# Kernel optimization log

Measured on AMD Instinct MI355X. Metric: run time of the kernel, lower is better.

Reference implementation:

```python
import jax, jax.numpy as jnp
import numpy as np

N = 50000
E = 800000
NODE_F = 128
HID = 96
TEMP_F = 10


def setup_inputs() -> dict:
    key = jax.random.key(0)
    ks = jax.random.split(key, 10)
    x = jax.random.normal(ks[0], (N, NODE_F), dtype=jnp.float32)
    edge_index = jax.random.randint(ks[1], (2, E), 0, N, dtype=jnp.int64)
    temporal = jax.random.normal(ks[2], (N, TEMP_F), dtype=jnp.float32)
    # GCNConv: lin weight [in, out] (no bias in lin), separate bias [out]
    W_gcn = jax.random.normal(ks[3], (NODE_F, HID), dtype=jnp.float32) / np.sqrt(NODE_F)
    b_gcn = jnp.zeros((HID,), dtype=jnp.float32)
    W1 = jax.random.normal(ks[4], (HID + TEMP_F, HID), dtype=jnp.float32) / np.sqrt(HID + TEMP_F)
    b1 = jax.random.normal(ks[5], (HID,), dtype=jnp.float32) * 0.01
    W2 = jax.random.normal(ks[6], (HID + NODE_F, 1), dtype=jnp.float32) / np.sqrt(HID + NODE_F)
    b2 = jax.random.normal(ks[7], (1,), dtype=jnp.float32) * 0.01
    return {"x": x, "edge_index": edge_index, "temporal": temporal,
            "W_gcn": W_gcn, "b_gcn": b_gcn, "W1": W1, "b1": b1, "W2": W2, "b2": b2}


def _gcn_conv(x, edge_index, W, b):
    n = x.shape[0]
    loop = jnp.arange(n, dtype=edge_index.dtype)
    src = jnp.concatenate([edge_index[0], loop])  # [E+N]
    dst = jnp.concatenate([edge_index[1], loop])
    # symmetric normalization with self-loops (PyG gcn_norm)
    ones = jnp.ones(src.shape[0], dtype=x.dtype)
    deg = jax.ops.segment_sum(ones, dst, num_segments=n)
    dinv = jnp.where(deg > 0, jax.lax.rsqrt(deg), 0.0)
    norm = dinv[src] * dinv[dst]  # [E+N]
    h = x @ W  # [N, HID]
    msg = h[src] * norm[:, None]  # [E+N, HID] gather + scale
    out = jax.ops.segment_sum(msg, dst, num_segments=n)  # scatter-add
    return out + b


def reference(x, edge_index, temporal, W_gcn, b_gcn, W1, b1, W2, b2):
    h = jax.nn.relu(_gcn_conv(x, edge_index, W_gcn, b_gcn))  # [N, HID]
    h = jnp.concatenate([h, temporal], axis=-1)              # [N, HID+TEMP_F]
    h = jax.nn.relu(h @ W1 + b1)                             # [N, HID]
    h = jnp.concatenate([h, x], axis=-1)                     # [N, HID+NODE_F]
    return jax.nn.relu(h @ W2 + b2)                          # [N, 1]
```

## Files before the change

### kernel.cpp

```cpp
#include <hip/hip_runtime.h>
#include <hip/hip_bf16.h>

#define NN 50000
#define NPAD 50048
#define NE 800000
#define NF 128
#define HH 96
#define TF 10
#define Z1DIM (HH + TF)
#define ZK 128
#define NCH 4
#define CW 24
#define NBK 196
#define CAP 5120
#define EPB 4096
#define FILLA_B ((NE + EPB - 1) / EPB)

typedef __attribute__((ext_vector_type(8))) short short8;
typedef __attribute__((ext_vector_type(8))) unsigned short ushort8;
typedef __attribute__((ext_vector_type(4))) float f32x4;

__device__ __forceinline__ float bu2f(unsigned short u) {
    union { unsigned int i; float f; } c;
    c.i = ((unsigned int)u) << 16;
    return c.f;
}
__device__ __forceinline__ unsigned short f2bu(float f) {
    union { __hip_bfloat16 h; unsigned short u; } c;
    c.h = __float2bfloat16(f);
    return c.u;
}

__global__ void k_init(int* __restrict__ bcur, int* __restrict__ off) {
    int t = threadIdx.x;
    if (t < NBK) bcur[t] = t * CAP;
    if (t == 255) off[NN] = NE;
}

#define WBLK (NF * HH / 4 / 256)
#define W1BLK (HH * ZK / 4 / 256)
#define ZTBLK (NPAD / 32)
#define ZPBLK 5
__global__ __launch_bounds__(256) void k_pre(const int* __restrict__ ei,
                                             int* __restrict__ bcur,
                                             int* __restrict__ temp,
                                             const float* __restrict__ W,
                                             const float* __restrict__ W1,
                                             const float* __restrict__ tmp,
                                             unsigned short* __restrict__ Wt,
                                             unsigned short* __restrict__ Wt1,
                                             unsigned short* __restrict__ zb) {
    const int t = threadIdx.x;
    if (blockIdx.x < FILLA_B) {
        __shared__ int hist[NBK], bas[NBK];
        for (int m = t; m < NBK; m += 256) hist[m] = 0;
        __syncthreads();
        const int e0 = blockIdx.x * EPB;
        const int ecap = min(e0 + EPB, NE);
        for (int e = e0 + t; e < ecap; e += 256) {
            int d = ei[NE + e];
            atomicAdd(&hist[d >> 8], 1);
        }
        __syncthreads();
        for (int m = t; m < NBK; m += 256) {
            int c = hist[m];
            bas[m] = c ? atomicAdd(&bcur[m], c) : 0;
            hist[m] = 0;
        }
        __syncthreads();
        for (int e = e0 + t; e < ecap; e += 256) {
            int d = ei[NE + e], s = ei[e];
            int b = d >> 8;
            int r = atomicAdd(&hist[b], 1);
            temp[bas[b] + r] = ((d & 255) << 16) | s;
        }
        return;
    }
    int b = blockIdx.x - FILLA_B;
    if (b < WBLK) {
        int e = (b * 256 + t) * 4;
        int n = e >> 7, k = e & 127;
        ushort4 v;
        v.x = f2bu(W[(k + 0) * HH + n]);
        v.y = f2bu(W[(k + 1) * HH + n]);
        v.z = f2bu(W[(k + 2) * HH + n]);
        v.w = f2bu(W[(k + 3) * HH + n]);
        *(ushort4*)(Wt + e) = v;
    } else if (b < WBLK + W1BLK) {
        int e = ((b - WBLK) * 256 + t) * 4;
        int n = e >> 7, k = e & 127;
        ushort4 v;
        v.x = (k + 0 < Z1DIM) ? f2bu(W1[(k + 0) * HH + n]) : (unsigned short)0;
        v.y = (k + 1 < Z1DIM) ? f2bu(W1[(k + 1) * HH + n]) : (unsigned short)0;
        v.z = (k + 2 < Z1DIM) ? f2bu(W1[(k + 2) * HH + n]) : (unsigned short)0;
        v.w = (k + 3 < Z1DIM) ? f2bu(W1[(k + 3) * HH + n]) : (unsigned short)0;
        *(ushort4*)(Wt1 + e) = v;
    } else if (b < WBLK + W1BLK + ZTBLK) {
        int t4 = ((b - WBLK - W1BLK) * 256 + t) * 4;
        int i = t4 >> 5, cc = t4 & 31;
        ushort4 v; v.x = v.y = v.z = v.w = 0;
        if (i < NN) {
            if (cc + 0 < TF) v.x = f2bu(tmp[(size_t)i * TF + cc + 0]);
            if (cc + 1 < TF) v.y = f2bu(tmp[(size_t)i * TF + cc + 1]);
            if (cc + 2 < TF) v.z = f2bu(tmp[(size_t)i * TF + cc + 2]);
            if (cc + 3 < TF) v.w = f2bu(tmp[(size_t)i * TF + cc + 3]);
        }
        *(ushort4*)(zb + (size_t)i * ZK + HH + cc) = v;
    } else {
        int t4 = ((b - WBLK - W1BLK - ZTBLK) * 256 + t) * 4;
        if (t4 < (NPAD - NN) * HH) {
            int i = NN + t4 / HH, j = t4 % HH;
            ushort4 z; z.x = z.y = z.z = z.w = 0;
            *(ushort4*)(zb + (size_t)i * ZK + j) = z;
        }
    }
}

__global__ __launch_bounds__(256) void k_off(const int* __restrict__ temp,
                                             const int* __restrict__ bcur,
                                             int* __restrict__ off) {
    __shared__ int ls[256], lc[256];
    const int b = blockIdx.x, t = threadIdx.x;
    int szt = (t < NBK) ? (bcur[t] - t * CAP) : 0;
    ls[t] = szt;
    __syncthreads();
#pragma unroll
    for (int d = 1; d < 256; d <<= 1) {
        int u = (t >= d) ? ls[t - d] : 0;
        __syncthreads();
        ls[t] += u;
        __syncthreads();
    }
    const int g0 = (b > 0) ? ls[b - 1] : 0;
    __syncthreads();
    ls[t] = 0;
    __syncthreads();
    const int seg0 = b * CAP;
    const int m = bcur[b] - seg0;
    for (int k = t; k < m; k += 256) atomicAdd(&ls[temp[seg0 + k] >> 16], 1);
    __syncthreads();
    const int myc = ls[t];
    lc[t] = myc;
    __syncthreads();
#pragma unroll
    for (int d = 1; d < 256; d <<= 1) {
        int u = (t >= d) ? lc[t - d] : 0;
        __syncthreads();
        lc[t] += u;
        __syncthreads();
    }
    const int i = b * 256 + t;
    if (i < NN) off[i] = g0 + lc[t] - myc;
}

__global__ __launch_bounds__(256) void k_gg(const int* __restrict__ temp,
                                            const int* __restrict__ bcur,
                                            unsigned short* __restrict__ csr,
                                            const int* __restrict__ off,
                                            const float* __restrict__ x,
                                            const unsigned short* __restrict__ Wt,
                                            const float* __restrict__ W2,
                                            unsigned short* __restrict__ hp_c,
                                            float* __restrict__ xw2) {
    const int t = threadIdx.x;
    if (blockIdx.x < NBK) {
        __shared__ int lc[256];
        const int b = blockIdx.x;
        const int i = b * 256 + t;
        lc[t] = (i < NN) ? off[i] : 0;
        __syncthreads();
        const int seg0 = b * CAP;
        const int m = bcur[b] - seg0;
        for (int k = t; k < m; k += 256) {
            int v = temp[seg0 + k];
            int r = atomicAdd(&lc[v >> 16], 1);
            csr[r] = (unsigned short)(v & 0xFFFF);
        }
        return;
    }
    const int wave = t >> 6;
    const int lane = t & 63;
    const int quad = lane >> 4;
    const int l16 = lane & 15;
    const int Mbase = (blockIdx.x - NBK) * 64 + wave * 16;
    const int row = Mbase + l16;
    const bool valid = row < NN;

    const float* xr = x + (size_t)row * NF + quad * 8;
    const unsigned short* brow = Wt + (size_t)l16 * NF + quad * 8;

    f32x4 acc[6] = {};
    float xs = 0.f;
#pragma unroll
    for (int ks = 0; ks < 4; ++ks) {
        short8 a = {};
        if (valid) {
            float4 f0 = *(const float4*)(xr + ks * 32);
            float4 f1 = *(const float4*)(xr + ks * 32 + 4);
            const float4 w0 = *(const float4*)(W2 + HH + quad * 8 + ks * 32);
            const float4 w1 = *(const float4*)(W2 + HH + quad * 8 + ks * 32 + 4);
            xs = fmaf(f0.x, w0.x, xs); xs = fmaf(f0.y, w0.y, xs);
            xs = fmaf(f0.z, w0.z, xs); xs = fmaf(f0.w, w0.w, xs);
            xs = fmaf(f1.x, w1.x, xs); xs = fmaf(f1.y, w1.y, xs);
            xs = fmaf(f1.z, w1.z, xs); xs = fmaf(f1.w, w1.w, xs);
            a[0] = (short)f2bu(f0.x); a[1] = (short)f2bu(f0.y);
            a[2] = (short)f2bu(f0.z); a[3] = (short)f2bu(f0.w);
            a[4] = (short)f2bu(f1.x); a[5] = (short)f2bu(f1.y);
            a[6] = (short)f2bu(f1.z); a[7] = (short)f2bu(f1.w);
        }
#pragma unroll
        for (int nt = 0; nt < 6; ++nt) {
            short8 bfrag = *(const short8*)(brow + (size_t)nt * 16 * NF + ks * 32);
            acc[nt] = __builtin_amdgcn_mfma_f32_16x16x32_bf16(a, bfrag, acc[nt], 0, 0, 0);
        }
    }
    xs += __shfl_xor(xs, 16, 64);
    xs += __shfl_xor(xs, 32, 64);
    if (quad == 0 && valid) xw2[row] = xs;

    const int r0 = Mbase + quad * 4;
    float dv[4];
#pragma unroll
    for (int k = 0; k < 4; ++k) {
        int r = r0 + k;
        dv[k] = (r < NN) ? rsqrtf((float)(off[r + 1] - off[r]) + 1.f) : 0.f;
    }
#pragma unroll
    for (int nt = 0; nt < 6; ++nt) {
        int n = nt * 16 + l16;
        int c = n / CW, jj = n - c * CW;
        unsigned short* dst = hp_c + (size_t)c * NN * CW + jj;
#pragma unroll
        for (int k = 0; k < 4; ++k)
            if (r0 + k < NN) dst[(size_t)(r0 + k) * CW] = f2bu(acc[nt][k] * dv[k]);
    }
}

#define RPC2 196
#define AGGB (8 * RPC2)
__global__ __launch_bounds__(256) void k_agg(const unsigned short* __restrict__ hp_c,
                                             const int* __restrict__ off,
                                             const unsigned short* __restrict__ csr,
                                             const float* __restrict__ bg,
                                             unsigned short* __restrict__ zb) {
    const int b = blockIdx.x;
    const int slot = b & 7;
    const int c = slot >> 1;
    const int r = (b >> 3) * 2 + (slot & 1);
    const int item = r * 256 + threadIdx.x;
    if (item >= NN * 2) return;
    const int i = item >> 1;
    const int h = item & 1;
    const unsigned short* __restrict__ base = hp_c + (size_t)c * NN * CW;

    float a[CW];
    if (h == 0) {
        const unsigned short* sp = base + (size_t)i * CW;
        ushort8 s0 = *(const ushort8*)(sp);
        ushort8 s1 = *(const ushort8*)(sp + 8);
        ushort8 s2 = *(const ushort8*)(sp + 16);
#pragma unroll
        for (int j = 0; j < 8; ++j) {
            a[j] = bu2f(s0[j]); a[8 + j] = bu2f(s1[j]); a[16 + j] = bu2f(s2[j]);
        }
    } else {
#pragma unroll
        for (int j = 0; j < CW; ++j) a[j] = 0.f;
    }

    const int start = off[i];
    const int end = off[i + 1];
    const int len = end - start;
    const float dv = rsqrtf((float)len + 1.f);
    const int half0 = (len + 1) >> 1;
    int k = h ? start + half0 : start;
    const int ke = h ? end : start + half0;
    for (; k + 1 < ke; k += 2) {
        const unsigned short* p0 = base + (size_t)csr[k] * CW;
        const unsigned short* p1 = base + (size_t)csr[k + 1] * CW;
        ushort8 v0 = *(const ushort8*)(p0);
        ushort8 v1 = *(const ushort8*)(p0 + 8);
        ushort8 v2 = *(const ushort8*)(p0 + 16);
        ushort8 w0 = *(const ushort8*)(p1);
        ushort8 w1 = *(const ushort8*)(p1 + 8);
        ushort8 w2 = *(const ushort8*)(p1 + 16);
#pragma unroll
        for (int j = 0; j < 8; ++j) {
            a[j]      += bu2f(v0[j]) + bu2f(w0[j]);
            a[8 + j]  += bu2f(v1[j]) + bu2f(w1[j]);
            a[16 + j] += bu2f(v2[j]) + bu2f(w2[j]);
        }
    }
    if (k < ke) {
        const unsigned short* p0 = base + (size_t)csr[k] * CW;
        ushort8 v0 = *(const ushort8*)(p0);
        ushort8 v1 = *(const ushort8*)(p0 + 8);
        ushort8 v2 = *(const ushort8*)(p0 + 16);
#pragma unroll
        for (int j = 0; j < 8; ++j) {
            a[j] += bu2f(v0[j]); a[8 + j] += bu2f(v1[j]); a[16 + j] += bu2f(v2[j]);
        }
    }
#pragma unroll
    for (int j = 0; j < CW; ++j) a[j] += __shfl_xor(a[j], 1, 64);
    if (h == 0) {
        const int j0 = c * CW;
        ushort8 o0, o1, o2;
#pragma unroll
        for (int j = 0; j < 8; ++j) {
            o0[j] = f2bu(fmaxf(fmaf(dv, a[j],      bg[j0 + j]),      0.f));
            o1[j] = f2bu(fmaxf(fmaf(dv, a[8 + j],  bg[j0 + 8 + j]),  0.f));
            o2[j] = f2bu(fmaxf(fmaf(dv, a[16 + j], bg[j0 + 16 + j]), 0.f));
        }
        unsigned short* zp = zb + (size_t)i * ZK + j0;
        *(ushort8*)(zp) = o0;
        *(ushort8*)(zp + 8) = o1;
        *(ushort8*)(zp + 16) = o2;
    }
}

__global__ __launch_bounds__(256) void k_mlp2(const unsigned short* __restrict__ zb,
                                              const unsigned short* __restrict__ Wt1,
                                              const float* __restrict__ b1,
                                              const float* __restrict__ W2,
                                              const float* __restrict__ b2,
                                              const float* __restrict__ xw2,
                                              float* __restrict__ out) {
    const int wave = threadIdx.x >> 6;
    const int lane = threadIdx.x & 63;
    const int quad = lane >> 4;
    const int l16 = lane & 15;
    const int Mbase = blockIdx.x * 64 + wave * 16;

    const unsigned short* arow = zb + (size_t)(Mbase + l16) * ZK + quad * 8;
    const unsigned short* brow = Wt1 + (size_t)l16 * ZK + quad * 8;

    f32x4 acc[6] = {};
#pragma unroll
    for (int ks = 0; ks < 4; ++ks) {
        short8 a = *(const short8*)(arow + ks * 32);
#pragma unroll
        for (int nt = 0; nt < 6; ++nt) {
            short8 bfrag = *(const short8*)(brow + (size_t)nt * 16 * ZK + ks * 32);
            acc[nt] = __builtin_amdgcn_mfma_f32_16x16x32_bf16(a, bfrag, acc[nt], 0, 0, 0);
        }
    }
    float bb[6], wa[6];
#pragma unroll
    for (int nt = 0; nt < 6; ++nt) {
        int c = nt * 16 + l16;
        bb[nt] = b1[c];
        wa[nt] = W2[c];
    }
    const float bias2 = b2[0];

#pragma unroll
    for (int reg = 0; reg < 4; ++reg) {
        const int r = Mbase + quad * 4 + reg;
        float p = 0.f;
#pragma unroll
        for (int nt = 0; nt < 6; ++nt)
            p = fmaf(fmaxf(acc[nt][reg] + bb[nt], 0.f), wa[nt], p);
#pragma unroll
        for (int m = 1; m < 16; m <<= 1) p += __shfl_xor(p, m, 64);
        if (l16 == 0 && r < NN) out[r] = fmaxf(p + xw2[r] + bias2, 0.f);
    }
}

extern "C" void kernel_launch(void* const* d_in, const int* in_sizes, int n_in,
                              void* d_out, int out_size, void* d_ws, size_t ws_size,
                              hipStream_t stream) {
    const float* x   = (const float*)d_in[0];
    const int*   ei  = (const int*)d_in[1];
    const float* tmp = (const float*)d_in[2];
    const float* Wg  = (const float*)d_in[3];
    const float* bg  = (const float*)d_in[4];
    const float* W1  = (const float*)d_in[5];
    const float* b1  = (const float*)d_in[6];
    const float* W2  = (const float*)d_in[7];
    const float* b2  = (const float*)d_in[8];
    float* out = (float*)d_out;

    char* base = (char*)d_ws;
    int* off  = (int*)base;
    int* bcur = (int*)(base + (256 << 10));
    unsigned short* csr = (unsigned short*)(base + (512 << 10));
    unsigned short* Wt  = (unsigned short*)(base + ((size_t)3 << 20));
    unsigned short* Wt1 = Wt + NF * HH;
    unsigned short* hp_c = (unsigned short*)(base + ((size_t)4 << 20));
    unsigned short* zb  = (unsigned short*)(base + ((size_t)14 << 20));
    float* xw2 = (float*)(base + ((size_t)27 << 20));
    int* temp  = (int*)(base + ((size_t)28 << 20));

    k_init <<<1, 256, 0, stream>>>(bcur, off);
    k_pre  <<<FILLA_B + WBLK + W1BLK + ZTBLK + ZPBLK, 256, 0, stream>>>(
                ei, bcur, temp, Wg, W1, tmp, Wt, Wt1, zb);
    k_off  <<<NBK, 256, 0, stream>>>(temp, bcur, off);
    k_gg   <<<NBK + NPAD / 64, 256, 0, stream>>>(temp, bcur, csr, off, x, Wt, W2, hp_c, xw2);
    k_agg  <<<AGGB, 256, 0, stream>>>(hp_c, off, csr, bg, zb);
    k_mlp2 <<<NPAD / 64, 256, 0, stream>>>(zb, Wt1, b1, W2, b2, xw2, out);
}
```

Baseline: 174.0 us.

## Pad feature chunks to 32 and split aggregation across 8 lanes per node

The per-chunk bf16 feature buffer is padded from 24 to 32 columns, so each node row is a 64-byte aligned segment. The aggregation kernel now gives each node 8 threads (4 column quarters times 2 edge halves) instead of 2, with each thread loading one 16-byte vector per neighbour. Neighbours are unrolled by 4, and the two halves are combined with a lane shuffle. This raises parallelism and cuts per-thread register use, at the cost of about a third more gather bytes for the padding quarter and more workspace, whose offsets are shifted.

```diff
diff --git a/kernel.cpp b/kernel.cpp
--- a/kernel.cpp
+++ b/kernel.cpp
@@ -11,6 +11,7 @@
 #define ZK 128
 #define NCH 4
 #define CW 24
+#define CWP 32
 #define NBK 196
 #define CAP 5120
 #define EPB 4096
@@ -229,15 +230,14 @@
     for (int nt = 0; nt < 6; ++nt) {
         int n = nt * 16 + l16;
         int c = n / CW, jj = n - c * CW;
-        unsigned short* dst = hp_c + (size_t)c * NN * CW + jj;
+        unsigned short* dst = hp_c + (size_t)c * NN * CWP + jj;
 #pragma unroll
         for (int k = 0; k < 4; ++k)
-            if (r0 + k < NN) dst[(size_t)(r0 + k) * CW] = f2bu(acc[nt][k] * dv[k]);
-    }
-}
-
-#define RPC2 196
-#define AGGB (8 * RPC2)
+            if (r0 + k < NN) dst[(size_t)(r0 + k) * CWP] = f2bu(acc[nt][k] * dv[k]);
+    }
+}
+
+#define AGGB (8 * 782)
 __global__ __launch_bounds__(256) void k_agg(const unsigned short* __restrict__ hp_c,
                                              const int* __restrict__ off,
                                              const unsigned short* __restrict__ csr,
@@ -248,24 +248,22 @@
     const int c = slot >> 1;
     const int r = (b >> 3) * 2 + (slot & 1);
     const int item = r * 256 + threadIdx.x;
-    if (item >= NN * 2) return;
-    const int i = item >> 1;
-    const int h = item & 1;
-    const unsigned short* __restrict__ base = hp_c + (size_t)c * NN * CW;
-
-    float a[CW];
+    if (item >= NN * 8) return;
+    const int i = item >> 3;
+    const int sub = item & 7;
+    const int q = sub & 3;
+    const int h = sub >> 2;
+    const int q8 = q * 8;
+    const unsigned short* __restrict__ base = hp_c + (size_t)c * NN * CWP + q8;
+
+    float a[8];
     if (h == 0) {
-        const unsigned short* sp = base + (size_t)i * CW;
-        ushort8 s0 = *(const ushort8*)(sp);
-        ushort8 s1 = *(const ushort8*)(sp + 8);
-        ushort8 s2 = *(const ushort8*)(sp + 16);
-#pragma unroll
-        for (int j = 0; j < 8; ++j) {
-            a[j] = bu2f(s0[j]); a[8 + j] = bu2f(s1[j]); a[16 + j] = bu2f(s2[j]);
-        }
+        ushort8 sv = *(const ushort8*)(base + (size_t)i * CWP);
+#pragma unroll
+        for (int j = 0; j < 8; ++j) a[j] = bu2f(sv[j]);
     } else {
 #pragma unroll
-        for (int j = 0; j < CW; ++j) a[j] = 0.f;
+        for (int j = 0; j < 8; ++j) a[j] = 0.f;
     }
 
     const int start = off[i];
@@ -275,47 +273,30 @@
     const int half0 = (len + 1) >> 1;
     int k = h ? start + half0 : start;
     const int ke = h ? end : start + half0;
-    for (; k + 1 < ke; k += 2) {
-        const unsigned short* p0 = base + (size_t)csr[k] * CW;
-        const unsigned short* p1 = base + (size_t)csr[k + 1] * CW;
-        ushort8 v0 = *(const ushort8*)(p0);
-        ushort8 v1 = *(const ushort8*)(p0 + 8);
-        ushort8 v2 = *(const ushort8*)(p0 + 16);
-        ushort8 w0 = *(const ushort8*)(p1);
-        ushort8 w1 = *(const ushort8*)(p1 + 8);
-        ushort8 w2 = *(const ushort8*)(p1 + 16);
-#pragma unroll
-        for (int j = 0; j < 8; ++j) {
-            a[j]      += bu2f(v0[j]) + bu2f(w0[j]);
-            a[8 + j]  += bu2f(v1[j]) + bu2f(w1[j]);
-            a[16 + j] += bu2f(v2[j]) + bu2f(w2[j]);
-        }
-    }
-    if (k < ke) {
-        const unsigned short* p0 = base + (size_t)csr[k] * CW;
-        ushort8 v0 = *(const ushort8*)(p0);
-        ushort8 v1 = *(const ushort8*)(p0 + 8);
-        ushort8 v2 = *(const ushort8*)(p0 + 16);
-#pragma unroll
-        for (int j = 0; j < 8; ++j) {
-            a[j] += bu2f(v0[j]); a[8 + j] += bu2f(v1[j]); a[16 + j] += bu2f(v2[j]);
-        }
-    }
-#pragma unroll
-    for (int j = 0; j < CW; ++j) a[j] += __shfl_xor(a[j], 1, 64);
-    if (h == 0) {
-        const int j0 = c * CW;
-        ushort8 o0, o1, o2;
-#pragma unroll
-        for (int j = 0; j < 8; ++j) {
-            o0[j] = f2bu(fmaxf(fmaf(dv, a[j],      bg[j0 + j]),      0.f));
-            o1[j] = f2bu(fmaxf(fmaf(dv, a[8 + j],  bg[j0 + 8 + j]),  0.f));
-            o2[j] = f2bu(fmaxf(fmaf(dv, a[16 + j], bg[j0 + 16 + j]), 0.f));
-        }
-        unsigned short* zp = zb + (size_t)i * ZK + j0;
-        *(ushort8*)(zp) = o0;
-        *(ushort8*)(zp + 8) = o1;
-        *(ushort8*)(zp + 16) = o2;
+    for (; k + 3 < ke; k += 4) {
+        int s0 = csr[k], s1 = csr[k + 1], s2 = csr[k + 2], s3 = csr[k + 3];
+        ushort8 v0 = *(const ushort8*)(base + (size_t)s0 * CWP);
+        ushort8 v1 = *(const ushort8*)(base + (size_t)s1 * CWP);
+        ushort8 v2 = *(const ushort8*)(base + (size_t)s2 * CWP);
+        ushort8 v3 = *(const ushort8*)(base + (size_t)s3 * CWP);
+#pragma unroll
+        for (int j = 0; j < 8; ++j)
+            a[j] += (bu2f(v0[j]) + bu2f(v1[j])) + (bu2f(v2[j]) + bu2f(v3[j]));
+    }
+    for (; k < ke; ++k) {
+        ushort8 v0 = *(const ushort8*)(base + (size_t)csr[k] * CWP);
+#pragma unroll
+        for (int j = 0; j < 8; ++j) a[j] += bu2f(v0[j]);
+    }
+#pragma unroll
+    for (int j = 0; j < 8; ++j) a[j] += __shfl_xor(a[j], 4, 64);
+    if (h == 0 && q < 3) {
+        const int j0 = c * CW + q8;
+        ushort8 o;
+#pragma unroll
+        for (int j = 0; j < 8; ++j)
+            o[j] = f2bu(fmaxf(fmaf(dv, a[j], bg[j0 + j]), 0.f));
+        *(ushort8*)(zb + (size_t)i * ZK + j0) = o;
     }
 }
 
@@ -388,9 +369,9 @@
     unsigned short* Wt  = (unsigned short*)(base + ((size_t)3 << 20));
     unsigned short* Wt1 = Wt + NF * HH;
     unsigned short* hp_c = (unsigned short*)(base + ((size_t)4 << 20));
-    unsigned short* zb  = (unsigned short*)(base + ((size_t)14 << 20));
-    float* xw2 = (float*)(base + ((size_t)27 << 20));
-    int* temp  = (int*)(base + ((size_t)28 << 20));
+    unsigned short* zb  = (unsigned short*)(base + ((size_t)17 << 20));
+    float* xw2 = (float*)(base + ((size_t)30 << 20));
+    int* temp  = (int*)(base + ((size_t)31 << 20));
 
     k_init <<<1, 256, 0, stream>>>(bcur, off);
     k_pre  <<<FILLA_B + WBLK + W1BLK + ZTBLK + ZPBLK, 256, 0, stream>>>(
```

Measured after the change: 169.1 us. 2.8% less time.
